# Performance work log

Measured on AMD Instinct MI355X. Metric: run time of the kernel, lower is better.

Reference implementation:

```python
import jax, jax.numpy as jnp
import numpy as np

H8, W8 = 64, 64
H4, W4 = 128, 128
C_LAT, C_HI = 256, 128
N_Q = 1024
ORIG_H, ORIG_W = 512, 512
NUM_ITERS = 4
TEMP = 20.0
DIM = 4 + C_HI + C_LAT        # 388 mixer output dim
IN_DIM = DIM + 3 * 49         # 535 mixer input dim
HID = 512


def _unit(v):
    return v / jnp.sqrt(jnp.maximum(jnp.sum(v * v, axis=-1, keepdims=True), 1e-12))


def setup_inputs() -> dict:
    key = jax.random.key(0)
    ks = jax.random.split(key, 20)
    fg = _unit(jax.random.normal(ks[0], (1, H8, W8, C_LAT), jnp.float32))
    hg = _unit(jax.random.normal(ks[1], (1, H4, W4, C_HI), jnp.float32))
    qf = _unit(jax.random.normal(ks[2], (1, N_Q, C_LAT), jnp.float32))
    hq = _unit(jax.random.normal(ks[3], (1, N_Q, C_HI), jnp.float32))
    p = lambda k, s, sc=0.05: sc * jax.random.normal(k, s, jnp.float32)
    return dict(
        feature_grid=fg, hires_feats_grid=hg, query_feats=qf, hires_query_feats=hq,
        hid1_w=p(ks[4], (16, 1, 3, 3)), hid1_b=jnp.zeros((16,), jnp.float32),
        hid2_w=p(ks[5], (1, 16, 3, 3)), hid2_b=jnp.zeros((1,), jnp.float32),
        hid3_w=p(ks[6], (32, 16, 3, 3)), hid3_b=jnp.zeros((32,), jnp.float32),
        hid4_w=p(ks[7], (32, 16)), hid4_b=jnp.zeros((16,), jnp.float32),
        occ_w=p(ks[8], (16, 2)), occ_b=jnp.zeros((2,), jnp.float32),
        mix_in_w=p(ks[9], (IN_DIM, HID), 0.02), mix_in_b=jnp.zeros((HID,), jnp.float32),
        mix_out_w=p(ks[10], (HID, DIM), 0.02), mix_out_b=jnp.zeros((DIM,), jnp.float32),
    )


def _conv2d(x, w, b, stride, pad):
    y = jax.lax.conv_general_dilated(x, w, (stride, stride), pad,
                                     dimension_numbers=('NCHW', 'OIHW', 'NCHW'))
    return y + b[None, :, None, None]


def _bilinear_sample(grid, coords):
    # grid [H,W,C]; coords [..., 2] as (y, x); edge-clamped bilinear gather.
    H, W = grid.shape[0], grid.shape[1]
    y, x = coords[..., 0], coords[..., 1]
    y0f, x0f = jnp.floor(y), jnp.floor(x)
    wy, wx = (y - y0f)[..., None], (x - x0f)[..., None]
    y0 = jnp.clip(y0f.astype(jnp.int32), 0, H - 1)
    y1 = jnp.clip(y0f.astype(jnp.int32) + 1, 0, H - 1)
    x0 = jnp.clip(x0f.astype(jnp.int32), 0, W - 1)
    x1 = jnp.clip(x0f.astype(jnp.int32) + 1, 0, W - 1)
    g00, g01 = grid[y0, x0], grid[y0, x1]
    g10, g11 = grid[y1, x0], grid[y1, x1]
    return (g00 * (1 - wy) * (1 - wx) + g01 * (1 - wy) * wx
            + g10 * wy * (1 - wx) + g11 * wy * wx)


def _forward(fg, hg, qf, hq, hid1_w, hid1_b, hid2_w, hid2_b, hid3_w, hid3_b,
             hid4_w, hid4_b, occ_w, occ_b, mix_in_w, mix_in_b, mix_out_w, mix_out_b):
    # --- tracks_from_cost_volume ---
    cv = jnp.einsum('bnc,bhwc->bnhw', qf, fg)                 # [1,N,64,64]
    b, n, h, w = cv.shape
    x = cv.reshape(b * n, 1, h, w)
    occ_map = jax.nn.relu(_conv2d(x, hid1_w, hid1_b, 1, 'SAME'))   # [bn,16,h,w]
    pmap = _conv2d(occ_map, hid2_w, hid2_b, 1, 'SAME').reshape(b * n, h * w)
    heat = jax.nn.softmax(pmap * TEMP, axis=-1).reshape(b * n, h, w)
    ey = jnp.einsum('bhw,h->b', heat, jnp.arange(h, dtype=jnp.float32))
    ex = jnp.einsum('bhw,w->b', heat, jnp.arange(w, dtype=jnp.float32))
    points = jnp.stack([ex * (ORIG_W / w), ey * (ORIG_H / h)], -1).reshape(b, n, 2)
    op = jnp.pad(occ_map, ((0, 0), (0, 0), (0, 2), (0, 2)))
    o3 = jax.nn.relu(_conv2d(op, hid3_w, hid3_b, 2, 'VALID'))
    o3 = o3.mean((-1, -2))                                     # [bn,32]
    o3 = jax.nn.relu(o3 @ hid4_w + hid4_b)
    o3 = (o3 @ occ_w + occ_b).reshape(b, n, 2)
    occ, expd = o3[..., 0], o3[..., 1]

    # --- iterative pips refinement ---
    cy, cx = jnp.meshgrid(jnp.arange(-3, 4), jnp.arange(-3, 4), indexing='ij')
    ctx = jnp.stack([cy, cx], -1).reshape(-1, 2).astype(jnp.float32)   # [49,2] (dy,dx)
    fg_avg = fg.reshape(1, H8 // 2, 2, W8 // 2, 2, C_LAT).mean((2, 4))
    pyramid = [hg, fg, fg_avg]
    feats = jnp.concatenate([hq, qf], -1)                      # [1,N,384]
    pos = points
    for it in range(NUM_ITERS):
        if it == 0:
            queries = [hq[0], qf[0], qf[0]]
        else:
            queries = [feats[0, :, :C_HI], feats[0, :, C_HI:], feats[0, :, C_HI:]]
        corrs = []
        for grid, q in zip(pyramid, queries):
            gh, gw = grid.shape[1], grid.shape[2]
            scale = jnp.array([gw / ORIG_W, gh / ORIG_H], jnp.float32)
            c = (pos[0] * scale)[:, ::-1]                      # (x,y)->(y,x), [N,2]
            coords2 = c[:, None, :] + ctx[None]                # [N,49,2]
            nb = _bilinear_sample(grid[0], coords2)            # [N,49,C]
            corrs.append(jnp.einsum('nsc,nc->ns', nb, q))
        corrs = jnp.concatenate(corrs, -1)[None]               # [1,N,147]
        mlp_in = jnp.concatenate([jnp.zeros_like(pos), occ[..., None],
                                  expd[..., None], feats, corrs], -1)
        res = jax.nn.gelu(mlp_in @ mix_in_w + mix_in_b) @ mix_out_w + mix_out_b
        pos = pos + res[..., :2]
        occ = occ + res[..., 2]
        expd = expd + res[..., 3]
        feats = feats + res[..., 4:]
    return jnp.concatenate([pos, occ[..., None], expd[..., None]], -1)  # [1,N,4]


def reference(feature_grid, hires_feats_grid, query_feats, hires_query_feats,
              hid1_w, hid1_b, hid2_w, hid2_b, hid3_w, hid3_b, hid4_w, hid4_b,
              occ_w, occ_b, mix_in_w, mix_in_b, mix_out_w, mix_out_b):
    return _forward(feature_grid, hires_feats_grid, query_feats, hires_query_feats,
                    hid1_w, hid1_b, hid2_w, hid2_b, hid3_w, hid3_b, hid4_w, hid4_b,
                    occ_w, occ_b, mix_in_w, mix_in_b, mix_out_w, mix_out_b)
```

## Files before the change

kernel.cpp:

```cpp
#include <hip/hip_runtime.h>
#include <hip/hip_bf16.h>
#include <math.h>


#define NQ 1024
#define TEMPF 20.0f
#define DIMV 388
#define INDIM 535
#define KPAD 544
#define HID 512

#define WS_CV      0
#define WS_FGAVG   (WS_CV + NQ*4096)
#define WS_POS     (WS_FGAVG + 262144)
#define WS_OCC     (WS_POS + NQ*2)
#define WS_EXPD    (WS_OCC + NQ)
#define WS_FEATS   (WS_EXPD + NQ)
#define WS_MLPIN   (WS_FEATS + NQ*384)
#define WS_HIDDEN  (WS_MLPIN + NQ*KPAD)
#define WS_W3B     (WS_HIDDEN + NQ*HID)
#define WS_PART    (WS_MLPIN + 278528)
#define WS_SUM3    WS_HIDDEN
#define WS_WIT     WS_CV
#define WS_WOT     (WS_CV + 139264)

#define OP 72
#define CVP 68

typedef __attribute__((ext_vector_type(8))) short bf16x8;
typedef __attribute__((ext_vector_type(4))) float f32x4;

__global__ __launch_bounds__(256) void k_prep_cv(
    const float* __restrict__ fg, const float* __restrict__ qf,
    const float* __restrict__ hq, const float* __restrict__ w3,
    float* __restrict__ ws) {
  __shared__ __hip_bfloat16 A_s[32 * 32];
  __shared__ __hip_bfloat16 B_s[64 * 32];
  const int bx = blockIdx.x;
  const int t = threadIdx.x;

  if (bx >= 2048) {
    int i = (bx - 2048) * 256 + t;
    if (i < 262144) {
      int c = i & 255, ox = (i >> 8) & 31, oy = i >> 13;
      const float* b = fg + (((oy * 2) * 64 + ox * 2) << 8) + c;
      ws[WS_FGAVG + i] = 0.25f * (b[0] + b[256] + b[16384] + b[16384 + 256]);
    } else if (i < 262144 + 393216) {
      int j = i - 262144;
      int n = j / 384, c = j - n * 384;
      ws[WS_FEATS + j] = (c < 128) ? hq[n * 128 + c] : qf[n * 256 + c - 128];
    } else if (i < 262144 + 393216 + 5120) {
      int j = i - (262144 + 393216);
      int e = j & 7, qd = (j >> 3) & 3, nl = (j >> 5) & 15;
      int nt = (j >> 9) & 1, kt = j >> 10;
      int k = kt * 32 + qd * 8 + e;
      int ic = k & 15, tap = k >> 4;
      int oc = nt * 16 + nl;
      float v = (tap < 9) ? w3[(oc * 16 + ic) * 9 + tap] : 0.f;
      ((__hip_bfloat16*)(ws + WS_W3B))[j] = __float2bfloat16(v);
    } else if (i < 262144 + 393216 + 5120 + 524288) {
      int j = i - (262144 + 393216 + 5120);
      ws[WS_SUM3 + j] = 0.f;
    }
    return;
  }

  const int wv = t >> 6, lane = t & 63;
  const int wm = wv & 1, wn = wv >> 1;
  const int quad = lane >> 4, nl = lane & 15;
  const int p0 = (bx & 63) * 64, m0 = (bx >> 6) * 32;
  f32x4 acc0 = {0.f, 0.f, 0.f, 0.f};
  f32x4 acc1 = {0.f, 0.f, 0.f, 0.f};

  for (int k0 = 0; k0 < 256; k0 += 32) {
    {
      int r = t >> 3, c = t & 7;
      float4 v = *(const float4*)&qf[(m0 + r) * 256 + k0 + c * 4];
      union { __hip_bfloat16 h[4]; uint2 u; } pk;
      pk.h[0] = __float2bfloat16(v.x); pk.h[1] = __float2bfloat16(v.y);
      pk.h[2] = __float2bfloat16(v.z); pk.h[3] = __float2bfloat16(v.w);
      *(uint2*)&A_s[r * 32 + c * 4] = pk.u;
    }
    {
      int r = t >> 2, c = t & 3;
      const float* src = &fg[(p0 + r) * 256 + k0 + c * 8];
      float4 v0 = *(const float4*)src;
      float4 v1 = *(const float4*)(src + 4);
      union { __hip_bfloat16 h[8]; uint4 u; } pk;
      pk.h[0] = __float2bfloat16(v0.x); pk.h[1] = __float2bfloat16(v0.y);
      pk.h[2] = __float2bfloat16(v0.z); pk.h[3] = __float2bfloat16(v0.w);
      pk.h[4] = __float2bfloat16(v1.x); pk.h[5] = __float2bfloat16(v1.y);
      pk.h[6] = __float2bfloat16(v1.z); pk.h[7] = __float2bfloat16(v1.w);
      *(uint4*)&B_s[r * 32 + c * 8] = pk.u;
    }
    __syncthreads();
    bf16x8 a = *(const bf16x8*)&A_s[(16 * wm + nl) * 32 + quad * 8];
    bf16x8 b0 = *(const bf16x8*)&B_s[(32 * wn + nl) * 32 + quad * 8];
    bf16x8 b1 = *(const bf16x8*)&B_s[(32 * wn + 16 + nl) * 32 + quad * 8];
    acc0 = __builtin_amdgcn_mfma_f32_16x16x32_bf16(a, b0, acc0, 0, 0, 0);
    acc1 = __builtin_amdgcn_mfma_f32_16x16x32_bf16(a, b1, acc1, 0, 0, 0);
    __syncthreads();
  }
#pragma unroll
  for (int nt = 0; nt < 2; nt++) {
    int n = p0 + 32 * wn + nt * 16 + nl;
#pragma unroll
    for (int r = 0; r < 4; r++) {
      int m = m0 + 16 * wm + quad * 4 + r;
      ws[WS_CV + m * 4096 + n] = (nt ? acc1[r] : acc0[r]);
    }
  }
}

__global__ __launch_bounds__(256, 5) void k_head_stripe(
    const float* __restrict__ h1w, const float* __restrict__ h1b,
    const float* __restrict__ h2w, const float* __restrict__ h2b,
    const float* __restrict__ h3b, float* __restrict__ ws) {
  __shared__ float cvs[8 * CVP];
  __shared__ float occ[6 * 16 * OP];

  const int bx = blockIdx.x;
  const int q = bx >> 4, st = bx & 15;
  const int y0 = st * 4;
  const int t = threadIdx.x;
  const int wv = t >> 6, lane = t & 63;
  const int role = (wv + bx) & 3;
  const float* cv = ws + WS_CV + q * 4096;

  if (t < 192) {
    int rc = t >> 1, side = t & 1;
    *(float4*)&occ[rc * OP + side * 68] = make_float4(0.f, 0.f, 0.f, 0.f);
  }
  if (st == 0 || st == 15) {
    int r = (st == 0) ? 0 : 5;
    for (int i = t; i < 16 * 18; i += 256)
      *(float4*)&occ[(r * 16 + (i / 18)) * OP + (i % 18) * 4] =
          make_float4(0.f, 0.f, 0.f, 0.f);
  }
#pragma unroll
  for (int j = 0; j < 2; j++) {
    int i = t + 256 * j;
    int lr = i >> 6, x = i & 63;
    int g = y0 - 2 + lr;
    cvs[lr * CVP + x + 1] = (g >= 0 && g < 64) ? cv[g * 64 + x] : 0.f;
  }
  if (t < 32) {
    int rr = t >> 2, c = t & 3;
    cvs[rr * CVP + ((c == 0) ? 0 : (64 + c))] = 0.f;
  }
  __syncthreads();

  {
    const int x = lane;
    const int chg = wv * 4;
    float w1r[4][9], b1r[4];
#pragma unroll
    for (int k = 0; k < 4; k++) {
      b1r[k] = h1b[chg + k];
#pragma unroll
      for (int j = 0; j < 9; j++) w1r[k][j] = h1w[(chg + k) * 9 + j];
    }
    for (int r = 0; r < 6; r++) {
      int yo = y0 - 1 + r;
      if (yo >= 0 && yo <= 63) {
        float p[9];
#pragma unroll
        for (int ky = 0; ky < 3; ky++) {
          const float* cp = &cvs[(r + ky) * CVP + x];
          p[3 * ky] = cp[0]; p[3 * ky + 1] = cp[1]; p[3 * ky + 2] = cp[2];
        }
#pragma unroll
        for (int k = 0; k < 4; k++) {
          float a = b1r[k];
#pragma unroll
          for (int j = 0; j < 9; j++) a += w1r[k][j] * p[j];
          occ[(r * 16 + chg + k) * OP + x + 4] = fmaxf(a, 0.f);
        }
      }
    }
  }
  __syncthreads();

  if (role == 1 || role == 2) {
    const __hip_bfloat16* W3B = (const __hip_bfloat16*)(ws + WS_W3B);
    const int oyl = role - 1;
    const int nl = lane & 15;
    const int qd = lane >> 4, qh = qd >> 1, ql = qd & 1;
    f32x4 acc00 = {0.f,0.f,0.f,0.f}, acc01 = {0.f,0.f,0.f,0.f};
    f32x4 acc10 = {0.f,0.f,0.f,0.f}, acc11 = {0.f,0.f,0.f,0.f};
#pragma unroll
    for (int kt = 0; kt < 5; kt++) {
      int tap = kt * 2 + qh;
      int tv = (tap < 9) ? tap : 0;
      int ky = (tv >= 6) ? 2 : ((tv >= 3) ? 1 : 0);
      int kx = tv - 3 * ky;
      const float* ap =
          &occ[((2 * oyl + 1 + ky) * 16 + ql * 8) * OP + 4 + kx + 2 * nl];
      union { bf16x8 v; __hip_bfloat16 h[8]; } a0u, a1u;
      if (tap < 9) {
#pragma unroll
        for (int j = 0; j < 8; j++) {
          a0u.h[j] = __float2bfloat16(ap[j * OP]);
          a1u.h[j] = __float2bfloat16(ap[j * OP + 32]);
        }
      } else {
#pragma unroll
        for (int j = 0; j < 8; j++) {
          a0u.h[j] = __float2bfloat16(0.f);
          a1u.h[j] = __float2bfloat16(0.f);
        }
      }
      bf16x8 b0 = *(const bf16x8*)&W3B[((kt * 2 + 0) * 16 + nl) * 32 + qd * 8];
      bf16x8 b1 = *(const bf16x8*)&W3B[((kt * 2 + 1) * 16 + nl) * 32 + qd * 8];
      acc00 = __builtin_amdgcn_mfma_f32_16x16x32_bf16(a0u.v, b0, acc00, 0, 0, 0);
      acc01 = __builtin_amdgcn_mfma_f32_16x16x32_bf16(a0u.v, b1, acc01, 0, 0, 0);
      acc10 = __builtin_amdgcn_mfma_f32_16x16x32_bf16(a1u.v, b0, acc10, 0, 0, 0);
      acc11 = __builtin_amdgcn_mfma_f32_16x16x32_bf16(a1u.v, b1, acc11, 0, 0, 0);
    }
    float bb0 = h3b[nl], bb1 = h3b[16 + nl];
    float s0 = 0.f, s1 = 0.f;
#pragma unroll
    for (int r = 0; r < 4; r++) {
      s0 += fmaxf(acc00[r] + bb0, 0.f) + fmaxf(acc10[r] + bb0, 0.f);
      s1 += fmaxf(acc01[r] + bb1, 0.f) + fmaxf(acc11[r] + bb1, 0.f);
    }
    s0 += __shfl_xor(s0, 16); s0 += __shfl_xor(s0, 32);
    s1 += __shfl_xor(s1, 16); s1 += __shfl_xor(s1, 32);
    if (lane < 16) {
      atomicAdd(&ws[WS_SUM3 + (q * 16 + st) * 32 + nl], s0);
      atomicAdd(&ws[WS_SUM3 + (q * 16 + st) * 32 + 16 + nl], s1);
    }
  } else {
    const int rl = ((role == 3) ? 2 : 0) + (lane >> 5);
    const int yg = y0 + rl;
    const int x0 = (lane & 31) * 2;
    float pa = 0.f, pb = 0.f;
    for (int ch = 0; ch < 16; ch++) {
#pragma unroll
      for (int ky = 0; ky < 3; ky++) {
        const float* bp = &occ[((rl + ky) * 16 + ch) * OP + x0];
        float f0 = bp[3];
        float2 fm = *(const float2*)(bp + 4);
        float f3 = bp[6];
        float wa = h2w[ch * 9 + 3 * ky], wb = h2w[ch * 9 + 3 * ky + 1],
              wc = h2w[ch * 9 + 3 * ky + 2];
        pa += wa * f0 + wb * fm.x + wc * fm.y;
        pb += wa * fm.x + wb * fm.y + wc * f3;
      }
    }
    float bb = h2b[0];
    float v0 = (pa + bb) * TEMPF, v1 = (pb + bb) * TEMPF;
    float mg = fmaxf(v0, v1);
#pragma unroll
    for (int off = 1; off < 64; off <<= 1) mg = fmaxf(mg, __shfl_xor(mg, off));
    float e0 = __expf(v0 - mg), e1 = __expf(v1 - mg);
    float s = e0 + e1;
    float sx = e0 * (float)x0 + e1 * (float)(x0 + 1);
    float sy = s * (float)yg;
#pragma unroll
    for (int off = 1; off < 64; off <<= 1) {
      s += __shfl_xor(s, off);
      sx += __shfl_xor(sx, off);
      sy += __shfl_xor(sy, off);
    }
    if (lane == 0) {
      int slot = q * 32 + st * 2 + ((role == 3) ? 1 : 0);
      *(float4*)&ws[WS_PART + slot * 4] = make_float4(mg, s, sx, sy);
    }
  }
}

__global__ __launch_bounds__(256) void k_merge_cvt(
    const float* __restrict__ w4, const float* __restrict__ b4,
    const float* __restrict__ w5, const float* __restrict__ b5,
    const float* __restrict__ wi, const float* __restrict__ wo,
    float* __restrict__ ws) {
  {
    int i = blockIdx.x * 256 + threadIdx.x;
    __hip_bfloat16* WIT = (__hip_bfloat16*)(ws + WS_WIT);
    __hip_bfloat16* WOT = (__hip_bfloat16*)(ws + WS_WOT);
    if (i < 278528) {
      int n = i / KPAD, k = i - n * KPAD;
      float v = (k < INDIM) ? wi[k * HID + n] : 0.f;
      WIT[i] = __float2bfloat16(v);
    } else if (i < 278528 + 229376) {
      int j = i - 278528;
      int n = j >> 9, k = j & 511;
      float v = (n < DIMV) ? wo[k * DIMV + n] : 0.f;
      WOT[j] = __float2bfloat16(v);
    }
  }
  if (blockIdx.x >= 256) return;

  __shared__ float sums_s[4][32];
  __shared__ float o4s[4][16];
  int t = threadIdx.x, wv = t >> 6, lane = t & 63;
  int q = blockIdx.x * 4 + wv;

  float M = -1e30f, S = 0.f, SX = 0.f, SY = 0.f;
  if (lane < 32) {
    float4 pv = *(const float4*)&ws[WS_PART + (q * 32 + lane) * 4];
    M = pv.x; S = pv.y; SX = pv.z; SY = pv.w;
  }
#pragma unroll
  for (int off = 1; off < 64; off <<= 1) {
    float Mo = __shfl_xor(M, off), So = __shfl_xor(S, off);
    float SXo = __shfl_xor(SX, off), SYo = __shfl_xor(SY, off);
    float Mn = fmaxf(M, Mo);
    float c1 = __expf(M - Mn), c2 = __expf(Mo - Mn);
    S = S * c1 + So * c2; SX = SX * c1 + SXo * c2; SY = SY * c1 + SYo * c2;
    M = Mn;
  }
  if (lane == 0) {
    ws[WS_POS + q * 2 + 0] = (SX / S) * 8.0f;
    ws[WS_POS + q * 2 + 1] = (SY / S) * 8.0f;
  }

  int ch = lane & 31, half = lane >> 5;
  float sm = 0.f;
#pragma unroll
  for (int s8 = 0; s8 < 8; s8++)
    sm += ws[WS_SUM3 + (q * 16 + half * 8 + s8) * 32 + ch];
  sm += __shfl_xor(sm, 32);
  if (lane < 32) sums_s[wv][lane] = sm * (1.f / 1024.f);
  __syncthreads();
  if (lane < 16) {
    float a = b4[lane];
#pragma unroll
    for (int i = 0; i < 32; i++) a += sums_s[wv][i] * w4[i * 16 + lane];
    o4s[wv][lane] = fmaxf(a, 0.f);
  }
  __syncthreads();
  if (lane < 2) {
    float r = b5[lane];
#pragma unroll
    for (int j = 0; j < 16; j++) r += o4s[wv][j] * w5[j * 2 + lane];
    if (lane == 0) ws[WS_OCC + q] = r;
    else           ws[WS_EXPD + q] = r;
  }
}

__global__ __launch_bounds__(256) void k_corr(
    const float* __restrict__ fg, const float* __restrict__ hg,
    float* __restrict__ ws) {
  __shared__ float qs[384];
  __shared__ float dbuf[3][64];
  int t = threadIdx.x;
  int wv = t >> 6, lane = t & 63;
  int cl = lane & 15, sub = lane >> 4;
  int n = blockIdx.x;
  const float* feats = ws + WS_FEATS + n * 384;
  float posx = ws[WS_POS + n * 2 + 0];
  float posy = ws[WS_POS + n * 2 + 1];
  __hip_bfloat16* mi = (__hip_bfloat16*)(ws + WS_MLPIN) + n * KPAD;

  for (int col = t; col < 384; col += 256) {
    float v = feats[col];
    qs[col] = v;
    mi[4 + col] = __float2bfloat16(v);
  }
  if (t < 4) {
    float v = (t == 2) ? ws[WS_OCC + n] : ((t == 3) ? ws[WS_EXPD + n] : 0.f);
    mi[t] = __float2bfloat16(v);
  }
  __syncthreads();

  float4 qh0 = *(const float4*)&qs[cl * 4];
  float4 qh1 = *(const float4*)&qs[64 + cl * 4];
  float4 qq0 = *(const float4*)&qs[128 + cl * 4];
  float4 qq1 = *(const float4*)&qs[192 + cl * 4];
  float4 qq2 = *(const float4*)&qs[256 + cl * 4];
  float4 qq3 = *(const float4*)&qs[320 + cl * 4];

#pragma unroll
  for (int L = 0; L < 3; L++) {
    const float* grid;
    int Hg, Wg;
    float scl;
    if (L == 0)      { grid = hg;             Hg = 128; Wg = 128; scl = 0.25f; }
    else if (L == 1) { grid = fg;             Hg = 64;  Wg = 64;  scl = 0.125f; }
    else             { grid = ws + WS_FGAVG;  Hg = 32;  Wg = 32;  scl = 0.0625f; }
    float cy = posy * scl, cx = posx * scl;
    int iy = (int)floorf(cy), ix = (int)floorf(cx);
#pragma unroll
    for (int g = 0; g < 4; g++) {
      int p = wv * 16 + g * 4 + sub;
      int a = p >> 3, b = p & 7;
      int row = iy + a - 3; row = row < 0 ? 0 : (row > Hg - 1 ? Hg - 1 : row);
      int col = ix + b - 3; col = col < 0 ? 0 : (col > Wg - 1 ? Wg - 1 : col);
      float acc;
      if (L == 0) {
        const float* gp = grid + (row * Wg + col) * 128 + cl * 4;
        float4 g0 = *(const float4*)gp;
        float4 g1 = *(const float4*)(gp + 64);
        acc = g0.x * qh0.x + g0.y * qh0.y + g0.z * qh0.z + g0.w * qh0.w +
              g1.x * qh1.x + g1.y * qh1.y + g1.z * qh1.z + g1.w * qh1.w;
      } else {
        const float* gp = grid + (row * Wg + col) * 256 + cl * 4;
        float4 g0 = *(const float4*)gp;
        float4 g1 = *(const float4*)(gp + 64);
        float4 g2 = *(const float4*)(gp + 128);
        float4 g3 = *(const float4*)(gp + 192);
        acc = g0.x * qq0.x + g0.y * qq0.y + g0.z * qq0.z + g0.w * qq0.w +
              g1.x * qq1.x + g1.y * qq1.y + g1.z * qq1.z + g1.w * qq1.w +
              g2.x * qq2.x + g2.y * qq2.y + g2.z * qq2.z + g2.w * qq2.w +
              g3.x * qq3.x + g3.y * qq3.y + g3.z * qq3.z + g3.w * qq3.w;
      }
      acc += __shfl_xor(acc, 1);
      acc += __shfl_xor(acc, 2);
      acc += __shfl_xor(acc, 4);
      acc += __shfl_xor(acc, 8);
      if (cl == 0) dbuf[L][p] = acc;
    }
  }
  __syncthreads();

  if (t < 147) {
    int L = t / 49, s = t - L * 49;
    int sa = s / 7, sb = s - sa * 7;
    float scl = (L == 0) ? 0.25f : ((L == 1) ? 0.125f : 0.0625f);
    float cy = posy * scl, cx = posx * scl;
    float wy = cy - floorf(cy), wx = cx - floorf(cx);
    int i00 = sa * 8 + sb;
    float d00 = dbuf[L][i00], d01 = dbuf[L][i00 + 1];
    float d10 = dbuf[L][i00 + 8], d11 = dbuf[L][i00 + 9];
    float corr = (1.f - wy) * (1.f - wx) * d00 + (1.f - wy) * wx * d01 +
                 wy * (1.f - wx) * d10 + wy * wx * d11;
    mi[388 + t] = __float2bfloat16(corr);
  }
}

__device__ __forceinline__ float gelu_tanh(float x) {
  float z = 0.7978845608028654f * (x + 0.044715f * x * x * x);
  z = fminf(fmaxf(z, -15.f), 15.f);
  float e = __expf(2.f * z);
  float th = (e - 1.f) / (e + 1.f);
  return 0.5f * x * (1.f + th);
}

__global__ __launch_bounds__(256) void k_mix1(
    const float* __restrict__ bias, float* __restrict__ ws) {
  __shared__ __hip_bfloat16 A_s[32 * 32];
  __shared__ __hip_bfloat16 B_s[32 * 32];
  const int t = threadIdx.x;
  const int wv = t >> 6, lane = t & 63;
  const int wm = wv & 1, wn = wv >> 1;
  const int quad = lane >> 4, nl = lane & 15;
  const int n0 = blockIdx.x * 32, m0 = blockIdx.y * 32;
  const unsigned short* Abf = (const unsigned short*)(ws + WS_MLPIN);
  const unsigned short* WIT = (const unsigned short*)(ws + WS_WIT);
  f32x4 acc = {0.f, 0.f, 0.f, 0.f};

  for (int k0 = 0; k0 < KPAD; k0 += 32) {
    if (t < 128) {
      int r = t >> 2, c = t & 3;
      *(uint4*)&A_s[r * 32 + c * 8] =
          *(const uint4*)&Abf[(m0 + r) * KPAD + k0 + c * 8];
    } else {
      int tt = t - 128;
      int r = tt >> 2, c = tt & 3;
      *(uint4*)&B_s[r * 32 + c * 8] =
          *(const uint4*)&WIT[(n0 + r) * KPAD + k0 + c * 8];
    }
    __syncthreads();
    bf16x8 a = *(const bf16x8*)&A_s[(16 * wm + nl) * 32 + quad * 8];
    bf16x8 b = *(const bf16x8*)&B_s[(16 * wn + nl) * 32 + quad * 8];
    acc = __builtin_amdgcn_mfma_f32_16x16x32_bf16(a, b, acc, 0, 0, 0);
    __syncthreads();
  }

  __hip_bfloat16* Hd = (__hip_bfloat16*)(ws + WS_HIDDEN);
  int nn = n0 + 16 * wn + nl;
  float bv = bias[nn];
#pragma unroll
  for (int r = 0; r < 4; r++) {
    int m = m0 + 16 * wm + quad * 4 + r;
    Hd[m * HID + nn] = __float2bfloat16(gelu_tanh(acc[r] + bv));
  }
}

__global__ __launch_bounds__(256) void k_mix2(
    const float* __restrict__ bias, float* __restrict__ ws,
    float* __restrict__ out) {
  __shared__ __hip_bfloat16 A_s[32 * 32];
  __shared__ __hip_bfloat16 B_s[32 * 32];
  const int t = threadIdx.x;
  const int wv = t >> 6, lane = t & 63;
  const int wm = wv & 1, wn = wv >> 1;
  const int quad = lane >> 4, nl = lane & 15;
  const int n0 = blockIdx.x * 32, m0 = blockIdx.y * 32;
  const unsigned short* Abf = (const unsigned short*)(ws + WS_HIDDEN);
  const unsigned short* WOT = (const unsigned short*)(ws + WS_WOT);
  f32x4 acc = {0.f, 0.f, 0.f, 0.f};

  for (int k0 = 0; k0 < HID; k0 += 32) {
    if (t < 128) {
      int r = t >> 2, c = t & 3;
      *(uint4*)&A_s[r * 32 + c * 8] =
          *(const uint4*)&Abf[(m0 + r) * HID + k0 + c * 8];
    } else {
      int tt = t - 128;
      int r = tt >> 2, c = tt & 3;
      *(uint4*)&B_s[r * 32 + c * 8] =
          *(const uint4*)&WOT[(n0 + r) * HID + k0 + c * 8];
    }
    __syncthreads();
    bf16x8 a = *(const bf16x8*)&A_s[(16 * wm + nl) * 32 + quad * 8];
    bf16x8 b = *(const bf16x8*)&B_s[(16 * wn + nl) * 32 + quad * 8];
    acc = __builtin_amdgcn_mfma_f32_16x16x32_bf16(a, b, acc, 0, 0, 0);
    __syncthreads();
  }

  int col = n0 + 16 * wn + nl;
  if (col < DIMV) {
    float bv = bias[col];
#pragma unroll
    for (int r = 0; r < 4; r++) {
      int m = m0 + 16 * wm + quad * 4 + r;
      float rr = acc[r] + bv;
      if (col < 2) {
        float v = ws[WS_POS + m * 2 + col] + rr;
        ws[WS_POS + m * 2 + col] = v;
        out[m * 4 + col] = v;
      } else if (col == 2) {
        float v = ws[WS_OCC + m] + rr;
        ws[WS_OCC + m] = v;
        out[m * 4 + 2] = v;
      } else if (col == 3) {
        float v = ws[WS_EXPD + m] + rr;
        ws[WS_EXPD + m] = v;
        out[m * 4 + 3] = v;
      } else {
        ws[WS_FEATS + m * 384 + (col - 4)] += rr;
      }
    }
  }
}

extern "C" void kernel_launch(void* const* d_in, const int* in_sizes, int n_in,
                              void* d_out, int out_size, void* d_ws, size_t ws_size,
                              hipStream_t stream) {
  const float* fg = (const float*)d_in[0];
  const float* hg = (const float*)d_in[1];
  const float* qf = (const float*)d_in[2];
  const float* hq = (const float*)d_in[3];
  const float* w1 = (const float*)d_in[4];
  const float* b1 = (const float*)d_in[5];
  const float* w2 = (const float*)d_in[6];
  const float* b2 = (const float*)d_in[7];
  const float* w3 = (const float*)d_in[8];
  const float* b3 = (const float*)d_in[9];
  const float* w4 = (const float*)d_in[10];
  const float* b4 = (const float*)d_in[11];
  const float* w5 = (const float*)d_in[12];
  const float* b5 = (const float*)d_in[13];
  const float* wi = (const float*)d_in[14];
  const float* bi = (const float*)d_in[15];
  const float* wo = (const float*)d_in[16];
  const float* bo = (const float*)d_in[17];
  float* ws = (float*)d_ws;
  float* out = (float*)d_out;

  k_prep_cv<<<6676, 256, 0, stream>>>(fg, qf, hq, w3, ws);
  k_head_stripe<<<16384, 256, 0, stream>>>(w1, b1, w2, b2, b3, ws);
  k_merge_cvt<<<1984, 256, 0, stream>>>(w4, b4, w5, b5, wi, wo, ws);
  for (int it = 0; it < 4; it++) {
    k_corr<<<1024, 256, 0, stream>>>(fg, hg, ws);
    k_mix1<<<dim3(16, 32), 256, 0, stream>>>(bi, ws);
    k_mix2<<<dim3(13, 32), 256, 0, stream>>>(bo, ws, out);
  }
}
```

Baseline: 310.5 us.

## Store cost volume and sampling grids in bf16, move mixer-input writes upstream

The cost volume is now written and read as bf16, halving its write/read traffic between the prep and head kernels. The feature grids (fine, coarse, pooled) are converted to bf16 copies once, so the per-iteration correlation kernel gathers half the bytes. The bf16 MLP input row for feats/occ/expd is written by the producers (prep, merge, mix2) rather than rebuilt in k_corr each iteration. The head conv also gains a sliding 3x3 window to reuse LDS reads. The cost is an extra conversion pass over the grids and lower precision in the correlations and the cost volume.

```diff
diff --git a/kernel.cpp b/kernel.cpp
--- a/kernel.cpp
+++ b/kernel.cpp
@@ -10,8 +10,13 @@
 #define KPAD 544
 #define HID 512
 
-#define WS_CV      0
-#define WS_FGAVG   (WS_CV + NQ*4096)
+#define WS_CVB     0
+#define WS_WIT     2097152
+#define WS_WOT     2236416
+#define WS_FG16    2351104
+#define WS_HG16    2875392
+#define WS_AV16    3923968
+#define WS_FGAVG   4194304
 #define WS_POS     (WS_FGAVG + 262144)
 #define WS_OCC     (WS_POS + NQ*2)
 #define WS_EXPD    (WS_OCC + NQ)
@@ -21,14 +26,14 @@
 #define WS_W3B     (WS_HIDDEN + NQ*HID)
 #define WS_PART    (WS_MLPIN + 278528)
 #define WS_SUM3    WS_HIDDEN
-#define WS_WIT     WS_CV
-#define WS_WOT     (WS_CV + 139264)
 
 #define OP 72
 #define CVP 68
 
 typedef __attribute__((ext_vector_type(8))) short bf16x8;
 typedef __attribute__((ext_vector_type(4))) float f32x4;
+
+union BU8 { uint4 u; __hip_bfloat16 h[8]; };
 
 __global__ __launch_bounds__(256) void k_prep_cv(
     const float* __restrict__ fg, const float* __restrict__ qf,
@@ -48,7 +53,14 @@
     } else if (i < 262144 + 393216) {
       int j = i - 262144;
       int n = j / 384, c = j - n * 384;
-      ws[WS_FEATS + j] = (c < 128) ? hq[n * 128 + c] : qf[n * 256 + c - 128];
+      float v = (c < 128) ? hq[n * 128 + c] : qf[n * 256 + c - 128];
+      ws[WS_FEATS + j] = v;
+      __hip_bfloat16* mi = (__hip_bfloat16*)(ws + WS_MLPIN);
+      mi[n * KPAD + 4 + c] = __float2bfloat16(v);
+      if (c == 0) {
+        mi[n * KPAD + 0] = __float2bfloat16(0.f);
+        mi[n * KPAD + 1] = __float2bfloat16(0.f);
+      }
     } else if (i < 262144 + 393216 + 5120) {
       int j = i - (262144 + 393216);
       int e = j & 7, qd = (j >> 3) & 3, nl = (j >> 5) & 15;
@@ -101,13 +113,14 @@
     acc1 = __builtin_amdgcn_mfma_f32_16x16x32_bf16(a, b1, acc1, 0, 0, 0);
     __syncthreads();
   }
+  __hip_bfloat16* cvb = (__hip_bfloat16*)ws;
 #pragma unroll
   for (int nt = 0; nt < 2; nt++) {
     int n = p0 + 32 * wn + nt * 16 + nl;
 #pragma unroll
     for (int r = 0; r < 4; r++) {
       int m = m0 + 16 * wm + quad * 4 + r;
-      ws[WS_CV + m * 4096 + n] = (nt ? acc1[r] : acc0[r]);
+      cvb[m * 4096 + n] = __float2bfloat16(nt ? acc1[r] : acc0[r]);
     }
   }
 }
@@ -125,7 +138,7 @@
   const int t = threadIdx.x;
   const int wv = t >> 6, lane = t & 63;
   const int role = (wv + bx) & 3;
-  const float* cv = ws + WS_CV + q * 4096;
+  const __hip_bfloat16* cvb = (const __hip_bfloat16*)ws + q * 4096;
 
   if (t < 192) {
     int rc = t >> 1, side = t & 1;
@@ -142,7 +155,8 @@
     int i = t + 256 * j;
     int lr = i >> 6, x = i & 63;
     int g = y0 - 2 + lr;
-    cvs[lr * CVP + x + 1] = (g >= 0 && g < 64) ? cv[g * 64 + x] : 0.f;
+    cvs[lr * CVP + x + 1] =
+        (g >= 0 && g < 64) ? __bfloat162float(cvb[g * 64 + x]) : 0.f;
   }
   if (t < 32) {
     int rr = t >> 2, c = t & 3;
@@ -160,20 +174,28 @@
 #pragma unroll
       for (int j = 0; j < 9; j++) w1r[k][j] = h1w[(chg + k) * 9 + j];
     }
+    float win[3][3];
+#pragma unroll
+    for (int j = 0; j < 3; j++) {
+      const float* cp = &cvs[j * CVP + x];
+      win[j][0] = cp[0]; win[j][1] = cp[1]; win[j][2] = cp[2];
+    }
     for (int r = 0; r < 6; r++) {
+      if (r > 0) {
+#pragma unroll
+        for (int c = 0; c < 3; c++) { win[0][c] = win[1][c]; win[1][c] = win[2][c]; }
+        const float* cp = &cvs[(r + 2) * CVP + x];
+        win[2][0] = cp[0]; win[2][1] = cp[1]; win[2][2] = cp[2];
+      }
       int yo = y0 - 1 + r;
       if (yo >= 0 && yo <= 63) {
-        float p[9];
-#pragma unroll
-        for (int ky = 0; ky < 3; ky++) {
-          const float* cp = &cvs[(r + ky) * CVP + x];
-          p[3 * ky] = cp[0]; p[3 * ky + 1] = cp[1]; p[3 * ky + 2] = cp[2];
-        }
 #pragma unroll
         for (int k = 0; k < 4; k++) {
           float a = b1r[k];
 #pragma unroll
-          for (int j = 0; j < 9; j++) a += w1r[k][j] * p[j];
+          for (int ky = 0; ky < 3; ky++)
+            a += w1r[k][3 * ky] * win[ky][0] + w1r[k][3 * ky + 1] * win[ky][1] +
+                 w1r[k][3 * ky + 2] * win[ky][2];
           occ[(r * 16 + chg + k) * OP + x + 4] = fmaxf(a, 0.f);
         }
       }
@@ -274,6 +296,7 @@
     const float* __restrict__ w4, const float* __restrict__ b4,
     const float* __restrict__ w5, const float* __restrict__ b5,
     const float* __restrict__ wi, const float* __restrict__ wo,
+    const float* __restrict__ fg, const float* __restrict__ hg,
     float* __restrict__ ws) {
   {
     int i = blockIdx.x * 256 + threadIdx.x;
@@ -283,11 +306,22 @@
       int n = i / KPAD, k = i - n * KPAD;
       float v = (k < INDIM) ? wi[k * HID + n] : 0.f;
       WIT[i] = __float2bfloat16(v);
-    } else if (i < 278528 + 229376) {
+    } else if (i < 507904) {
       int j = i - 278528;
       int n = j >> 9, k = j & 511;
       float v = (n < DIMV) ? wo[k * DIMV + n] : 0.f;
       WOT[j] = __float2bfloat16(v);
+    } else {
+      int j = i - 507904;
+      if (j < 1048576) {
+        ((__hip_bfloat16*)(ws + WS_FG16))[j] = __float2bfloat16(fg[j]);
+      } else if (j < 3145728) {
+        int k = j - 1048576;
+        ((__hip_bfloat16*)(ws + WS_HG16))[k] = __float2bfloat16(hg[k]);
+      } else if (j < 3407872) {
+        int k = j - 3145728;
+        ((__hip_bfloat16*)(ws + WS_AV16))[k] = __float2bfloat16(ws[WS_FGAVG + k]);
+      }
     }
   }
   if (blockIdx.x >= 256) return;
@@ -335,14 +369,13 @@
     float r = b5[lane];
 #pragma unroll
     for (int j = 0; j < 16; j++) r += o4s[wv][j] * w5[j * 2 + lane];
-    if (lane == 0) ws[WS_OCC + q] = r;
-    else           ws[WS_EXPD + q] = r;
-  }
-}
-
-__global__ __launch_bounds__(256) void k_corr(
-    const float* __restrict__ fg, const float* __restrict__ hg,
-    float* __restrict__ ws) {
+    __hip_bfloat16* mi = (__hip_bfloat16*)(ws + WS_MLPIN);
+    if (lane == 0) { ws[WS_OCC + q] = r;  mi[q * KPAD + 2] = __float2bfloat16(r); }
+    else           { ws[WS_EXPD + q] = r; mi[q * KPAD + 3] = __float2bfloat16(r); }
+  }
+}
+
+__global__ __launch_bounds__(256) void k_corr(float* __restrict__ ws) {
   __shared__ float qs[384];
   __shared__ float dbuf[3][64];
   int t = threadIdx.x;
@@ -354,32 +387,27 @@
   float posy = ws[WS_POS + n * 2 + 1];
   __hip_bfloat16* mi = (__hip_bfloat16*)(ws + WS_MLPIN) + n * KPAD;
 
-  for (int col = t; col < 384; col += 256) {
-    float v = feats[col];
-    qs[col] = v;
-    mi[4 + col] = __float2bfloat16(v);
-  }
-  if (t < 4) {
-    float v = (t == 2) ? ws[WS_OCC + n] : ((t == 3) ? ws[WS_EXPD + n] : 0.f);
-    mi[t] = __float2bfloat16(v);
-  }
+  for (int col = t; col < 384; col += 256) qs[col] = feats[col];
   __syncthreads();
 
-  float4 qh0 = *(const float4*)&qs[cl * 4];
-  float4 qh1 = *(const float4*)&qs[64 + cl * 4];
-  float4 qq0 = *(const float4*)&qs[128 + cl * 4];
-  float4 qq1 = *(const float4*)&qs[192 + cl * 4];
-  float4 qq2 = *(const float4*)&qs[256 + cl * 4];
-  float4 qq3 = *(const float4*)&qs[320 + cl * 4];
+  float qh[8], qq[16];
+#pragma unroll
+  for (int j = 0; j < 8; j++) qh[j] = qs[cl * 8 + j];
+#pragma unroll
+  for (int j = 0; j < 16; j++) qq[j] = qs[128 + cl * 16 + j];
+
+  const __hip_bfloat16* G0 = (const __hip_bfloat16*)(ws + WS_HG16);
+  const __hip_bfloat16* G1 = (const __hip_bfloat16*)(ws + WS_FG16);
+  const __hip_bfloat16* G2 = (const __hip_bfloat16*)(ws + WS_AV16);
 
 #pragma unroll
   for (int L = 0; L < 3; L++) {
-    const float* grid;
+    const __hip_bfloat16* grid;
     int Hg, Wg;
     float scl;
-    if (L == 0)      { grid = hg;             Hg = 128; Wg = 128; scl = 0.25f; }
-    else if (L == 1) { grid = fg;             Hg = 64;  Wg = 64;  scl = 0.125f; }
-    else             { grid = ws + WS_FGAVG;  Hg = 32;  Wg = 32;  scl = 0.0625f; }
+    if (L == 0)      { grid = G0; Hg = 128; Wg = 128; scl = 0.25f; }
+    else if (L == 1) { grid = G1; Hg = 64;  Wg = 64;  scl = 0.125f; }
+    else             { grid = G2; Hg = 32;  Wg = 32;  scl = 0.0625f; }
     float cy = posy * scl, cx = posx * scl;
     int iy = (int)floorf(cy), ix = (int)floorf(cx);
 #pragma unroll
@@ -388,23 +416,21 @@
       int a = p >> 3, b = p & 7;
       int row = iy + a - 3; row = row < 0 ? 0 : (row > Hg - 1 ? Hg - 1 : row);
       int col = ix + b - 3; col = col < 0 ? 0 : (col > Wg - 1 ? Wg - 1 : col);
-      float acc;
+      float acc = 0.f;
       if (L == 0) {
-        const float* gp = grid + (row * Wg + col) * 128 + cl * 4;
-        float4 g0 = *(const float4*)gp;
-        float4 g1 = *(const float4*)(gp + 64);
-        acc = g0.x * qh0.x + g0.y * qh0.y + g0.z * qh0.z + g0.w * qh0.w +
-              g1.x * qh1.x + g1.y * qh1.y + g1.z * qh1.z + g1.w * qh1.w;
+        BU8 g0; g0.u = *(const uint4*)(grid + (row * Wg + col) * 128 + cl * 8);
+#pragma unroll
+        for (int j = 0; j < 8; j++) acc += __bfloat162float(g0.h[j]) * qh[j];
       } else {
-        const float* gp = grid + (row * Wg + col) * 256 + cl * 4;
-        float4 g0 = *(const float4*)gp;
-        float4 g1 = *(const float4*)(gp + 64);
-        float4 g2 = *(const float4*)(gp + 128);
-        float4 g3 = *(const float4*)(gp + 192);
-        acc = g0.x * qq0.x + g0.y * qq0.y + g0.z * qq0.z + g0.w * qq0.w +
-              g1.x * qq1.x + g1.y * qq1.y + g1.z * qq1.z + g1.w * qq1.w +
-              g2.x * qq2.x + g2.y * qq2.y + g2.z * qq2.z + g2.w * qq2.w +
-              g3.x * qq3.x + g3.y * qq3.y + g3.z * qq3.z + g3.w * qq3.w;
+        const __hip_bfloat16* gp = grid + (row * Wg + col) * 256 + cl * 16;
+        BU8 g0, g1;
+        g0.u = *(const uint4*)gp;
+        g1.u = *(const uint4*)(gp + 8);
+#pragma unroll
+        for (int j = 0; j < 8; j++) {
+          acc += __bfloat162float(g0.h[j]) * qq[j];
+          acc += __bfloat162float(g1.h[j]) * qq[8 + j];
+        }
       }
       acc += __shfl_xor(acc, 1);
       acc += __shfl_xor(acc, 2);
@@ -514,6 +540,7 @@
   int col = n0 + 16 * wn + nl;
   if (col < DIMV) {
     float bv = bias[col];
+    __hip_bfloat16* mib = (__hip_bfloat16*)(ws + WS_MLPIN);
 #pragma unroll
     for (int r = 0; r < 4; r++) {
       int m = m0 + 16 * wm + quad * 4 + r;
@@ -526,12 +553,16 @@
         float v = ws[WS_OCC + m] + rr;
         ws[WS_OCC + m] = v;
         out[m * 4 + 2] = v;
+        mib[m * KPAD + 2] = __float2bfloat16(v);
       } else if (col == 3) {
         float v = ws[WS_EXPD + m] + rr;
         ws[WS_EXPD + m] = v;
         out[m * 4 + 3] = v;
+        mib[m * KPAD + 3] = __float2bfloat16(v);
       } else {
-        ws[WS_FEATS + m * 384 + (col - 4)] += rr;
+        float v = ws[WS_FEATS + m * 384 + (col - 4)] + rr;
+        ws[WS_FEATS + m * 384 + (col - 4)] = v;
+        mib[m * KPAD + col] = __float2bfloat16(v);
       }
     }
   }
@@ -563,9 +594,9 @@
 
   k_prep_cv<<<6676, 256, 0, stream>>>(fg, qf, hq, w3, ws);
   k_head_stripe<<<16384, 256, 0, stream>>>(w1, b1, w2, b2, b3, ws);
-  k_merge_cvt<<<1984, 256, 0, stream>>>(w4, b4, w5, b5, wi, wo, ws);
+  k_merge_cvt<<<15296, 256, 0, stream>>>(w4, b4, w5, b5, wi, wo, fg, hg, ws);
   for (int it = 0; it < 4; it++) {
-    k_corr<<<1024, 256, 0, stream>>>(fg, hg, ws);
+    k_corr<<<1024, 256, 0, stream>>>(ws);
     k_mix1<<<dim3(16, 32), 256, 0, stream>>>(bi, ws);
     k_mix2<<<dim3(13, 32), 256, 0, stream>>>(bo, ws, out);
   }
```

Measured after the change: 309.2 us. No clear change (-0.4%).
